# Optimization experiments

Hardware: AMD Instinct MI355X
Metric: run time of the kernel (lower is better)

The kernel has to match this reference:

```python
import jax, jax.numpy as jnp
import numpy as np

B, S, D, H, NS = 4, 2048, 1024, 16, 300
DK = D // H                      # 64
NSP = (NS + H - 1) // H * H      # 304 (padded skills)
DG = NSP // H                    # 19
NEG_FILL = -1e9                  # fp32 path in the torch module


def setup_inputs() -> dict:
    key = jax.random.key(0)
    ks = jax.random.split(key, 12)
    sc = 0.02
    return {
        "context_sequence": jax.random.normal(ks[0], (B, S, D), jnp.float32),
        "value_sequence": jax.random.normal(ks[1], (B, S, NS), jnp.float32),
        "mask": jnp.triu(jnp.ones((S, S), jnp.bool_), k=1),  # causal: True = masked
        # weights stored as [in, out] (math-equivalent to torch's x @ W.T + b)
        "Wq": jax.random.normal(ks[2], (D, D), jnp.float32) * sc,
        "bq": jnp.zeros((D,), jnp.float32),
        "Wk": jax.random.normal(ks[3], (D, D), jnp.float32) * sc,
        "bk": jnp.zeros((D,), jnp.float32),
        "Wv": jax.random.normal(ks[4], (NS, NS), jnp.float32) * sc,
        "bv": jnp.zeros((NS,), jnp.float32),
        "Wg": jax.random.normal(ks[5], (NS, D), jnp.float32) * sc,  # gain_to_context
        "bg": jnp.zeros((D,), jnp.float32),
        "Wo": jax.random.normal(ks[6], (D, D), jnp.float32) * sc,   # output_proj
        "bo": jnp.zeros((D,), jnp.float32),
    }


def reference(context_sequence, value_sequence, mask,
              Wq, bq, Wk, bk, Wv, bv, Wg, bg, Wo, bo):
    b = context_sequence.shape[0]
    orig_dtype = context_sequence.dtype

    # Q, K: [b, H, S, DK]
    Q = (context_sequence @ Wq + bq).reshape(b, -1, H, DK).transpose(0, 2, 1, 3)
    K = (context_sequence @ Wk + bk).reshape(b, -1, H, DK).transpose(0, 2, 1, 3)

    # intrinsic-gain V: project in skill space, zero-pad to NSP, split heads -> [b, H, S, DG]
    V_proj = value_sequence @ Wv + bv
    V_proj = jnp.pad(V_proj, ((0, 0), (0, 0), (0, NSP - NS)))
    V = V_proj.reshape(b, -1, H, DG).transpose(0, 2, 1, 3)

    # fp32 score upcast, scale by sqrt(d_k), mask, cast back, softmax
    scores = jnp.einsum('bhqd,bhkd->bhqk',
                        Q.astype(jnp.float32), K.astype(jnp.float32)) / np.sqrt(DK)
    scores = jnp.where(mask, NEG_FILL, scores).astype(orig_dtype)
    attn = jax.nn.softmax(scores, axis=-1)

    # [b, H, S, DG] -> [b, S, NSP] -> slice to NS
    head_gains = jnp.einsum('bhqk,bhkd->bhqd', attn, V)
    agg = head_gains.transpose(0, 2, 1, 3).reshape(b, -1, NSP)[..., :NS]

    output = agg @ Wg + bg            # gain_to_context
    return output @ Wo + bo           # output_proj (dropout is identity in eval)
```

## Files before the change

kernel.cpp:

```cpp
#include <hip/hip_runtime.h>
#include <hip/hip_bf16.h>

#define MROWS 8192
#define DMODEL 1024
#define SLEN 2048
#define NHEADS 16
#define DKH 64
#define DGH 19
#define NSKILL 300
#define KGPAD 320
#define AGG_LD 320
#define QK_LD 2048
#define VK 320
#define VTN 384

typedef __attribute__((ext_vector_type(8))) short short8;
typedef __attribute__((ext_vector_type(4))) float floatx4;

__device__ __forceinline__ float bf2f(unsigned short u) {
  union { unsigned int i; float f; } cv;
  cv.i = ((unsigned int)u) << 16;
  return cv.f;
}
__device__ __forceinline__ unsigned short f2bf(float f) {
  __hip_bfloat16 h = __float2bfloat16(f);
  unsigned short u;
  __builtin_memcpy(&u, &h, 2);
  return u;
}

__device__ __forceinline__ float exp2hw(float x) {
#if __has_builtin(__builtin_amdgcn_exp2f)
  return __builtin_amdgcn_exp2f(x);
#else
  return __expf(x * 0.6931471805599453f);
#endif
}
__device__ __forceinline__ unsigned int cvt_pk_bf16(float lo, float hi) {
  unsigned int r;
  asm("v_cvt_pk_bf16_f32 %0, %1, %2" : "=v"(r) : "v"(lo), "v"(hi));
  return r;
}

__device__ __forceinline__ void ld8(const float* p, float* v) {
  float4 a = *(const float4*)p;
  float4 b = *((const float4*)p + 1);
  v[0]=a.x; v[1]=a.y; v[2]=a.z; v[3]=a.w;
  v[4]=b.x; v[5]=b.y; v[6]=b.z; v[7]=b.w;
}
__device__ __forceinline__ void st1(float* p, float v) { *p = v; }
__device__ __forceinline__ void st1(__hip_bfloat16* p, float v) {
  unsigned short raw = f2bf(v); __builtin_memcpy(p, &raw, 2);
}
__device__ __forceinline__ void st8(__hip_bfloat16* p, const float* v) {
  ushort4 a, b;
  a.x=f2bf(v[0]); a.y=f2bf(v[1]); a.z=f2bf(v[2]); a.w=f2bf(v[3]);
  b.x=f2bf(v[4]); b.y=f2bf(v[5]); b.z=f2bf(v[6]); b.w=f2bf(v[7]);
  *(ushort4*)p = a;
  *((ushort4*)p + 1) = b;
}

__device__ __forceinline__ void gl_lds16(const void* g, void* l) {
  __builtin_amdgcn_global_load_lds(
      (const __attribute__((address_space(1))) unsigned int*)g,
      (__attribute__((address_space(3))) unsigned int*)l, 16, 0, 0);
}

__global__ __launch_bounds__(256)
void prep_mega_kernel(const float* __restrict__ X,
                      const float* __restrict__ Vin,
                      const float* __restrict__ Wg,
                      const float* __restrict__ bq, const float* __restrict__ bk,
                      const float* __restrict__ bv,
                      const float* __restrict__ Wq, const float* __restrict__ Wk,
                      const float* __restrict__ Wo, const float* __restrict__ Wv,
                      __hip_bfloat16* __restrict__ Xb,
                      __hip_bfloat16* __restrict__ Vb16,
                      __hip_bfloat16* __restrict__ Wgb,
                      float* __restrict__ biasqk, float* __restrict__ biasv,
                      float* __restrict__ z384,
                      __hip_bfloat16* __restrict__ Wtqk,
                      __hip_bfloat16* __restrict__ WoT,
                      __hip_bfloat16* __restrict__ Wvt)
{
  const int bid = blockIdx.x;
  const int t = threadIdx.x;
  if (bid < 8192) {
    int i = (bid * 256 + t) * 4;
    float4 v = *(const float4*)(X + i);
    ushort4 s;
    s.x = f2bf(v.x); s.y = f2bf(v.y); s.z = f2bf(v.z); s.w = f2bf(v.w);
    *(ushort4*)((__hip_bfloat16*)Xb + i) = s;
    return;
  }
  if (bid < 9472) {
    int idx = (bid - 8192) * 256 + t;
    int row = idx / 40;
    int c8  = (idx - row * 40) * 8;
    const float* ip = Vin + (size_t)row * NSKILL + c8;
    float v[8];
    if (c8 + 8 <= NSKILL) {
      ld8(ip, v);
    } else {
      #pragma unroll
      for (int u = 0; u < 8; u++)
        v[u] = (c8 + u < NSKILL) ? ip[u] : 0.f;
    }
    st8(Vb16 + (size_t)row * VK + c8, v);
    return;
  }
  if (bid < 9856) {
    int i4 = ((bid - 9472) * 256 + t) * 4;
    int r = i4 >> 10;
    ushort4 s = {0, 0, 0, 0};
    if (r < NSKILL) {
      float4 v = *(const float4*)(Wg + i4);
      s.x = f2bf(v.x); s.y = f2bf(v.y); s.z = f2bf(v.z); s.w = f2bf(v.w);
    }
    *(ushort4*)((__hip_bfloat16*)Wgb + i4) = s;
    return;
  }
  if (bid == 9856) {
    for (int i = t; i < 1024; i += 256) { biasqk[i] = bq[i]; biasqk[1024 + i] = bk[i]; }
    for (int i = t; i < 384; i += 256) {
      biasv[i] = (i < NSKILL) ? bv[i] : 0.f;
      z384[i] = 0.f;
    }
    return;
  }
  const float* W; __hip_bfloat16* Wt; int K, Nld, Ntrue, Kpad, kx, ny;
  if (bid < 10881)      { int l = bid - 9857;  W=Wq; Wt=Wtqk;            K=1024; Nld=1024; Ntrue=1024; Kpad=1024; kx=l&31; ny=l>>5; }
  else if (bid < 11905) { int l = bid - 10881; W=Wk; Wt=Wtqk+1024*1024;  K=1024; Nld=1024; Ntrue=1024; Kpad=1024; kx=l&31; ny=l>>5; }
  else if (bid < 12929) { int l = bid - 11905; W=Wo; Wt=WoT;             K=1024; Nld=1024; Ntrue=1024; Kpad=1024; kx=l&31; ny=l>>5; }
  else                  { int l = bid - 12929; W=Wv; Wt=Wvt;             K=NSKILL; Nld=NSKILL; Ntrue=NSKILL; Kpad=VK; kx=l%10; ny=l/10; }
  __shared__ float tb[32][33];
  const int k0 = kx * 32;
  const int n0 = ny * 32;
  const int tx = t & 31, ty = t >> 5;
  #pragma unroll
  for (int i = 0; i < 4; i++) {
    int k = k0 + ty + i*8;
    int nn = n0 + tx;
    tb[ty + i*8][tx] = (k < K && nn < Ntrue) ? W[(size_t)k * Nld + nn] : 0.f;
  }
  __syncthreads();
  #pragma unroll
  for (int i = 0; i < 4; i++) {
    int nn = n0 + ty + i*8;
    int kk = k0 + tx;
    st1(Wt + (size_t)nn * Kpad + kk, tb[tx][ty + i*8]);
  }
}

__device__ __forceinline__ void gemm_core(const short* __restrict__ Ag,
                                          const short* __restrict__ Bg,
                                          int lda, int ldb, int K,
                                          int m0, int n0,
                                          short* Al, short* Bl,
                                          int tid, floatx4 (&acc)[4][4])
{
  const int lane = tid & 63;
  const int wave = tid >> 6;
  const int wy = wave >> 1, wx = wave & 1;
  const int n = lane & 15;
  const int quad = lane >> 4;

  for (int k0 = 0; k0 < K; k0 += 64) {
    #pragma unroll
    for (int it = 0; it < 4; it++) {
      int ci = it*256 + tid;
      int r = ci >> 3, c = ci & 7;
      int cs = c ^ (r & 7);
      gl_lds16(Ag + (size_t)(m0 + r) * lda + k0 + cs*8, &Al[ci*8]);
    }
    #pragma unroll
    for (int it = 0; it < 4; it++) {
      int ci = it*256 + tid;
      int r = ci >> 3, c = ci & 7;
      int cs = c ^ (r & 7);
      gl_lds16(Bg + (size_t)(n0 + r) * ldb + k0 + cs*8, &Bl[ci*8]);
    }
    __syncthreads();

    #pragma unroll
    for (int s = 0; s < 2; s++) {
      short8 af[4], bfr[4];
      const int c = s*4 + quad;
      #pragma unroll
      for (int i = 0; i < 4; i++) {
        int r = wy*64 + i*16 + n;
        af[i] = *(const short8*)&Al[(r*8 + (c ^ (r & 7)))*8];
      }
      #pragma unroll
      for (int j = 0; j < 4; j++) {
        int r = wx*64 + j*16 + n;
        bfr[j] = *(const short8*)&Bl[(r*8 + (c ^ (r & 7)))*8];
      }
      #pragma unroll
      for (int i = 0; i < 4; i++)
        #pragma unroll
        for (int j = 0; j < 4; j++)
          acc[i][j] = __builtin_amdgcn_mfma_f32_16x16x32_bf16(af[i], bfr[j], acc[i][j], 0, 0, 0);
    }
    __syncthreads();
  }
}

__global__ __launch_bounds__(256)
void gemm_qk_vt_kernel(const __hip_bfloat16* __restrict__ Xb,
                       const __hip_bfloat16* __restrict__ Wtqk,
                       const float* __restrict__ biasqk,
                       __hip_bfloat16* __restrict__ QKbuf,
                       const __hip_bfloat16* __restrict__ Vb16,
                       const __hip_bfloat16* __restrict__ Wvt,
                       const float* __restrict__ biasv,
                       __hip_bfloat16* __restrict__ VT)
{
  __shared__ __align__(16) short Al[128*64];
  __shared__ __align__(16) short Bl[128*64];
  const int tid = threadIdx.x;
  const int lane = tid & 63;
  const int wave = tid >> 6;
  const int wy = wave >> 1, wx = wave & 1;
  const int n = lane & 15;
  const int quad = lane >> 4;

  floatx4 acc[4][4];
  #pragma unroll
  for (int i = 0; i < 4; i++)
    #pragma unroll
    for (int j = 0; j < 4; j++) acc[i][j] = (floatx4){0.f,0.f,0.f,0.f};

  if (blockIdx.x < 1024) {
    const int bx = blockIdx.x & 15, by = blockIdx.x >> 4;
    const int m0 = by * 128, n0 = bx * 128;
    gemm_core((const short*)Xb, (const short*)Wtqk, DMODEL, DMODEL, DMODEL,
              m0, n0, Al, Bl, tid, acc);
    float bj[4];
    #pragma unroll
    for (int j = 0; j < 4; j++) bj[j] = biasqk[n0 + wx*64 + j*16 + n];
    #pragma unroll
    for (int i = 0; i < 4; i++) {
      #pragma unroll
      for (int r = 0; r < 4; r++) {
        int row = m0 + wy*64 + i*16 + quad*4 + r;
        __hip_bfloat16* cp = QKbuf + (size_t)row * QK_LD;
        #pragma unroll
        for (int j = 0; j < 4; j++) {
          int col = n0 + wx*64 + j*16 + n;
          st1(cp + col, acc[i][j][r] + bj[j]);
        }
      }
    }
  } else {
    const int l = blockIdx.x - 1024;
    const int bx = l % 3, by = l / 3;
    const int m0 = by * 128, n0 = bx * 128;
    gemm_core((const short*)Vb16, (const short*)Wvt, VK, VK, VK,
              m0, n0, Al, Bl, tid, acc);
    float bj[4];
    #pragma unroll
    for (int j = 0; j < 4; j++) bj[j] = biasv[n0 + wx*64 + j*16 + n];
    #pragma unroll
    for (int i = 0; i < 4; i++) {
      int row0 = m0 + wy*64 + i*16 + quad*4;
      int bb = row0 >> 11, rin = row0 & 2047;
      #pragma unroll
      for (int j = 0; j < 4; j++) {
        int col = n0 + wx*64 + j*16 + n;
        ushort4 pk;
        pk.x = f2bf(acc[i][j][0] + bj[j]);
        pk.y = f2bf(acc[i][j][1] + bj[j]);
        pk.z = f2bf(acc[i][j][2] + bj[j]);
        pk.w = f2bf(acc[i][j][3] + bj[j]);
        *(ushort4*)(VT + ((size_t)bb * VTN + col) * SLEN + rin) = pk;
      }
    }
  }
}

__global__ __launch_bounds__(256)
void wgo_bgo_kernel(const __hip_bfloat16* __restrict__ WoT,
                    const __hip_bfloat16* __restrict__ Wgb,
                    const float* __restrict__ z384,
                    __hip_bfloat16* __restrict__ WgoT,
                    const float* __restrict__ bg, const float* __restrict__ Wo,
                    const float* __restrict__ bo, float* __restrict__ bgo)
{
  __shared__ __align__(16) short Al[128*64];
  __shared__ __align__(16) short Bl[128*64];
  const int tid = threadIdx.x;
  if (blockIdx.x < 24) {
    const int lane = tid & 63;
    const int wave = tid >> 6;
    const int wy = wave >> 1, wx = wave & 1;
    const int n = lane & 15;
    const int quad = lane >> 4;
    const int bx = blockIdx.x % 3, by = blockIdx.x / 3;
    const int m0 = by * 128, n0 = bx * 128;
    floatx4 acc[4][4];
    #pragma unroll
    for (int i = 0; i < 4; i++)
      #pragma unroll
      for (int j = 0; j < 4; j++) acc[i][j] = (floatx4){0.f,0.f,0.f,0.f};
    gemm_core((const short*)WoT, (const short*)Wgb, DMODEL, DMODEL, DMODEL,
              m0, n0, Al, Bl, tid, acc);
    float bj[4];
    #pragma unroll
    for (int j = 0; j < 4; j++) bj[j] = z384[n0 + wx*64 + j*16 + n];
    #pragma unroll
    for (int i = 0; i < 4; i++) {
      #pragma unroll
      for (int r = 0; r < 4; r++) {
        int row = m0 + wy*64 + i*16 + quad*4 + r;
        __hip_bfloat16* cp = WgoT + (size_t)row * 384;
        #pragma unroll
        for (int j = 0; j < 4; j++) {
          int col = n0 + wx*64 + j*16 + n;
          st1(cp + col, acc[i][j][r] + bj[j]);
        }
      }
    }
  } else {
    __shared__ float red[256];
    const int c   = tid & 15;
    const int jg  = tid >> 4;
    const int col = (blockIdx.x - 24) * 16 + c;
    float acc = 0.f;
    const int j0 = jg * 64;
    #pragma unroll 8
    for (int j = j0; j < j0 + 64; j++)
      acc = fmaf(bg[j], Wo[(size_t)j * DMODEL + col], acc);
    red[tid] = acc;
    __syncthreads();
    if (jg == 0) {
      float s = 0.f;
      #pragma unroll
      for (int g = 0; g < 16; g++) s += red[g*16 + c];
      bgo[col] = s + bo[col];
    }
  }
}

__global__ __launch_bounds__(256)
void gemm_final_kernel(const __hip_bfloat16* __restrict__ A,
                       const __hip_bfloat16* __restrict__ Bt,
                       const float* __restrict__ bias,
                       float* __restrict__ C)
{
  __shared__ __align__(16) short Al[128*64];
  __shared__ __align__(16) short Bl[128*64];
  const int tid = threadIdx.x;
  const int lane = tid & 63;
  const int wave = tid >> 6;
  const int wy = wave >> 1, wx = wave & 1;
  const int n = lane & 15;
  const int quad = lane >> 4;
  const int m0 = blockIdx.y * 128;
  const int n0 = blockIdx.x * 128;
  floatx4 acc[4][4];
  #pragma unroll
  for (int i = 0; i < 4; i++)
    #pragma unroll
    for (int j = 0; j < 4; j++) acc[i][j] = (floatx4){0.f,0.f,0.f,0.f};
  gemm_core((const short*)A, (const short*)Bt, KGPAD, 384, KGPAD,
            m0, n0, Al, Bl, tid, acc);
  float bj[4];
  #pragma unroll
  for (int j = 0; j < 4; j++) bj[j] = bias[n0 + wx*64 + j*16 + n];
  #pragma unroll
  for (int i = 0; i < 4; i++) {
    #pragma unroll
    for (int r = 0; r < 4; r++) {
      int row = m0 + wy*64 + i*16 + quad*4 + r;
      float* cp = C + (size_t)row * DMODEL;
      #pragma unroll
      for (int j = 0; j < 4; j++) {
        int col = n0 + wx*64 + j*16 + n;
        cp[col] = acc[i][j][r] + bj[j];
      }
    }
  }
}

#define ATT_BM 128
#define ATT_BK 64
#define ATT_GRID (24*64)

__global__ __launch_bounds__(256)
void attn_mfma_kernel(const __hip_bfloat16* __restrict__ Qb,
                      const __hip_bfloat16* __restrict__ Kb,
                      const __hip_bfloat16* __restrict__ VTg,
                      __hip_bfloat16* __restrict__ Agg,
                      float* __restrict__ Pm, float* __restrict__ Pl,
                      float* __restrict__ Po)
{
  __shared__ __align__(16) short Kf[2][64*64];
  __shared__ __align__(16) short Vf[2][32*64];
  __shared__ __align__(16) unsigned int Plds[4][2][2][4][16][4];

  const int tid  = threadIdx.x;
  const int lane = tid & 63;
  const int wave = tid >> 6;
  const int n    = lane & 15;
  const int quad = lane >> 4;

  const int cid = blockIdx.x >> 6;
  const int bh  = blockIdx.x & 63;
  const int h   = bh & 15;
  const int b   = bh >> 4;
  int qt, kt0, nt, mode;
  if (cid == 0)      { qt = 7;       kt0 = 0;  nt = 16; mode = 0; }
  else if (cid <= 8) { qt = cid + 7; kt0 = 0;  nt = 16; mode = 1; }
  else if (cid == 9) { qt = 15;      kt0 = 16; nt = 16; mode = 2; }
  else {
    int e = (cid - 10) >> 1;
    if (((cid - 10) & 1) == 0) { qt = 6 - e;  kt0 = 0;  nt = 14 - 2*e; mode = 0; }
    else                       { qt = 14 - e; kt0 = 16; nt = 14 - 2*e; mode = 2; }
  }
  const int qbase = qt * ATT_BM;
  const size_t bS = (size_t)b * SLEN;

  const float QSCALE = 0.18033688f;
  short8 qf[2][2];
  #pragma unroll
  for (int rf = 0; rf < 2; rf++)
    #pragma unroll
    for (int ks = 0; ks < 2; ks++) {
      const __hip_bfloat16* qp = Qb + (bS + qbase + wave*32 + rf*16 + n) * QK_LD
                                    + h*DKH + ks*32 + quad*8;
      short8 v = *(const short8*)qp;
      #pragma unroll
      for (int e = 0; e < 8; e++) {
        float f = bf2f((unsigned short)v[e]) * QSCALE;
        v[e] = (short)f2bf(f);
      }
      qf[rf][ks] = v;
    }

  const short* kp;
  {
    int f = tid;
    int nn = f & 15, q = (f >> 4) & 3, c = (f >> 6) & 3;
    kp = (const short*)Kb + (bS + kt0*64 + c*16 + nn) * QK_LD + h*DKH + q*8;
  }
  const short* vp;
  {
    int g = tid;
    int vn = g & 15, vq = (g >> 4) & 3, sv = (g >> 6) & 1, cv = g >> 7;
    vp = (const short*)VTg + ((size_t)b * VTN + h*DGH + cv*16 + vn) * SLEN
         + kt0*64 + sv*32 + vq*8;
  }

  floatx4 of[2][2];
  float mrow[2], lrow[2];
  #pragma unroll
  for (int rf = 0; rf < 2; rf++) {
    #pragma unroll
    for (int cv = 0; cv < 2; cv++) of[rf][cv] = (floatx4){0.f,0.f,0.f,0.f};
    mrow[rf] = -1e30f; lrow[rf] = 0.f;
  }

  const int wrow_max = qbase + wave*32 + 31;

  auto stage = [&](int buf) {
    gl_lds16(kp,      &Kf[buf][tid*8]);
    gl_lds16(kp + 32, &Kf[buf][(tid + 256)*8]);
    gl_lds16(vp,      &Vf[buf][tid*8]);
    kp += 64 * QK_LD;
    vp += 64;
  };

  auto compute_tile = [&](int buf, int kbase) {
    if (kbase > wrow_max) return;
    short8 kfr[4][2];
    #pragma unroll
    for (int cf = 0; cf < 4; cf++)
      #pragma unroll
      for (int s = 0; s < 2; s++)
        kfr[cf][s] = *(const short8*)&Kf[buf][((s*4 + cf)*64 + lane)*8];

    floatx4 sf[2][4];
    __builtin_amdgcn_s_setprio(1);
    #pragma unroll
    for (int rf = 0; rf < 2; rf++)
      #pragma unroll
      for (int cf = 0; cf < 4; cf++) {
        floatx4 a2 = (floatx4){0.f,0.f,0.f,0.f};
        a2 = __builtin_amdgcn_mfma_f32_16x16x32_bf16(kfr[cf][0], qf[rf][0], a2, 0, 0, 0);
        a2 = __builtin_amdgcn_mfma_f32_16x16x32_bf16(kfr[cf][1], qf[rf][1], a2, 0, 0, 0);
        sf[rf][cf] = a2;
      }
    __builtin_amdgcn_s_setprio(0);

    #pragma unroll
    for (int rf = 0; rf < 2; rf++) {
      const int qrow = qbase + wave*32 + rf*16 + n;
      if (kbase + 63 > qbase + wave*32 + rf*16) {
        #pragma unroll
        for (int cf = 0; cf < 4; cf++)
          #pragma unroll
          for (int r = 0; r < 4; r++) {
            int key = kbase + cf*16 + quad*4 + r;
            if (key > qrow) sf[rf][cf][r] = -INFINITY;
          }
      }
      float m0 = fmaxf(sf[rf][0][0], sf[rf][0][1]);
      #pragma unroll
      for (int i = 2; i < 16; i += 2)
        m0 = fmaxf(fmaxf(m0, sf[rf][i>>2][i&3]), sf[rf][(i+1)>>2][(i+1)&3]);
      m0 = fmaxf(m0, __shfl_xor(m0, 16));
      m0 = fmaxf(m0, __shfl_xor(m0, 32));
      float mnew = fmaxf(mrow[rf], m0);
      float alpha = exp2hw(mrow[rf] - mnew);
      mrow[rf] = mnew;
      float rs = 0.f;
      #pragma unroll
      for (int cf = 0; cf < 4; cf++)
        #pragma unroll
        for (int r = 0; r < 4; r++) {
          float p = exp2hw(sf[rf][cf][r] - mnew);
          sf[rf][cf][r] = p;
          rs += p;
        }
      rs += __shfl_xor(rs, 16);
      rs += __shfl_xor(rs, 32);
      lrow[rf] = lrow[rf] * alpha + rs;
      #pragma unroll
      for (int cv = 0; cv < 2; cv++)
        #pragma unroll
        for (int r = 0; r < 4; r++) of[rf][cv][r] *= alpha;

      #pragma unroll
      for (int cf = 0; cf < 4; cf++) {
        unsigned int w0 = cvt_pk_bf16(sf[rf][cf][0], sf[rf][cf][1]);
        unsigned int w1 = cvt_pk_bf16(sf[rf][cf][2], sf[rf][cf][3]);
        int s   = cf >> 1;
        int qt2 = 2*(cf & 1) + (quad >> 1);
        int jp  = 2*(quad & 1);
        *(uint2*)&Plds[wave][rf][s][qt2][n][jp] = make_uint2(w0, w1);
      }
    }

    short8 vfr[2][2];
    #pragma unroll
    for (int cv = 0; cv < 2; cv++)
      #pragma unroll
      for (int s = 0; s < 2; s++)
        vfr[cv][s] = *(const short8*)&Vf[buf][((cv*2 + s)*64 + lane)*8];

    __builtin_amdgcn_s_setprio(1);
    #pragma unroll
    for (int rf = 0; rf < 2; rf++) {
      short8 p0 = *(const short8*)&Plds[wave][rf][0][quad][n][0];
      short8 p1 = *(const short8*)&Plds[wave][rf][1][quad][n][0];
      #pragma unroll
      for (int cv = 0; cv < 2; cv++) {
        floatx4 a2 = of[rf][cv];
        a2 = __builtin_amdgcn_mfma_f32_16x16x32_bf16(vfr[cv][0], p0, a2, 0, 0, 0);
        a2 = __builtin_amdgcn_mfma_f32_16x16x32_bf16(vfr[cv][1], p1, a2, 0, 0, 0);
        of[rf][cv] = a2;
      }
    }
    __builtin_amdgcn_s_setprio(0);
  };

  stage(0);
  for (int kt = 0; kt < nt; kt += 2) {
    stage(1);
    asm volatile("s_waitcnt vmcnt(3)" ::: "memory");
    __builtin_amdgcn_s_barrier();
    __builtin_amdgcn_sched_barrier(0);
    compute_tile(0, (kt0 + kt) * ATT_BK);
    __builtin_amdgcn_sched_barrier(0);
    __builtin_amdgcn_s_barrier();

    if (kt + 2 < nt) {
      stage(0);
      asm volatile("s_waitcnt vmcnt(3)" ::: "memory");
    } else {
      asm volatile("s_waitcnt vmcnt(0)" ::: "memory");
    }
    __builtin_amdgcn_s_barrier();
    __builtin_amdgcn_sched_barrier(0);
    compute_tile(1, (kt0 + kt + 1) * ATT_BK);
    __builtin_amdgcn_sched_barrier(0);
    __builtin_amdgcn_s_barrier();
  }

  if (mode == 0) {
    #pragma unroll
    for (int rf = 0; rf < 2; rf++) {
      float inv = 1.f / lrow[rf];
      int row = qbase + wave*32 + rf*16 + n;
      __hip_bfloat16* op = Agg + (bS + row)*AGG_LD + h*DGH;
      #pragma unroll
      for (int cv = 0; cv < 2; cv++)
        #pragma unroll
        for (int r = 0; r < 4; r++) {
          int dim = cv*16 + quad*4 + r;
          if (dim < DGH) st1(op + dim, of[rf][cv][r] * inv);
        }
    }
    if (h == 15) {
      int row = qbase + (tid >> 1);
      int c0 = 304 + (tid & 1) * 8;
      float z[8] = {0.f,0.f,0.f,0.f,0.f,0.f,0.f,0.f};
      st8(Agg + (bS + row)*AGG_LD + c0, z);
    }
  } else {
    const int p = (qt - 8) * 64 + bh;
    const int sl = mode - 1;
    #pragma unroll
    for (int rf = 0; rf < 2; rf++) {
      int rowl = wave*32 + rf*16 + n;
      size_t ri = (size_t)(sl*512 + p)*128 + rowl;
      float* po = Po + ri*20;
      #pragma unroll
      for (int cv = 0; cv < 2; cv++)
        #pragma unroll
        for (int r = 0; r < 4; r++) {
          int dim = cv*16 + quad*4 + r;
          if (dim < DGH) po[dim] = of[rf][cv][r];
        }
      if (quad == 0) { Pm[ri] = mrow[rf]; Pl[ri] = lrow[rf]; }
    }
  }
}

__global__ __launch_bounds__(256)
void attn_combine_kernel(const float* __restrict__ Pm, const float* __restrict__ Pl,
                         const float* __restrict__ Po,
                         __hip_bfloat16* __restrict__ Agg)
{
  int idx = blockIdx.x * 256 + threadIdx.x;
  int p = idx >> 7, rowl = idx & 127;
  int qt = 8 + (p >> 6), bh = p & 63, h = bh & 15, b = bh >> 4;
  size_t riA = (size_t)p*128 + rowl;
  size_t riB = (size_t)(512 + p)*128 + rowl;
  float mA = Pm[riA], mB = Pm[riB];
  float lA = Pl[riA], lB = Pl[riB];
  float m = fmaxf(mA, mB);
  float wA = exp2hw(mA - m), wB = exp2hw(mB - m);
  float inv = 1.f / (wA*lA + wB*lB);
  wA *= inv; wB *= inv;
  const float* oA = Po + riA*20;
  const float* oB = Po + riB*20;
  size_t row = (size_t)b*SLEN + qt*128 + rowl;
  __hip_bfloat16* op = Agg + row*AGG_LD + h*DGH;
  #pragma unroll
  for (int d = 0; d < DGH; d++)
    st1(op + d, wA*oA[d] + wB*oB[d]);
  if (h == 15) {
    uint4 z = {0,0,0,0};
    *(uint4*)(Agg + row*AGG_LD + 304) = z;
    *(uint4*)(Agg + row*AGG_LD + 312) = z;
  }
}

extern "C" void kernel_launch(void* const* d_in, const int* in_sizes, int n_in,
                              void* d_out, int out_size, void* d_ws, size_t ws_size,
                              hipStream_t stream) {
  const float* X   = (const float*)d_in[0];
  const float* Vin = (const float*)d_in[1];
  const float* Wq  = (const float*)d_in[3];
  const float* bq  = (const float*)d_in[4];
  const float* Wk  = (const float*)d_in[5];
  const float* bk  = (const float*)d_in[6];
  const float* Wv  = (const float*)d_in[7];
  const float* bv  = (const float*)d_in[8];
  const float* Wg  = (const float*)d_in[9];
  const float* bg  = (const float*)d_in[10];
  const float* Wo  = (const float*)d_in[11];
  const float* bo  = (const float*)d_in[12];
  float* out = (float*)d_out;

  char* ws = (char*)d_ws;
  __hip_bfloat16* Xb    = (__hip_bfloat16*)(ws);
  __hip_bfloat16* AggB  = (__hip_bfloat16*)(ws);
  __hip_bfloat16* WgoT  = (__hip_bfloat16*)(ws + 12582912);
  float*          bgoW  = (float*)         (ws + 13369344);
  __hip_bfloat16* QKbuf = (__hip_bfloat16*)(ws + 16777216);
  __hip_bfloat16* WoT   = (__hip_bfloat16*)(ws + 50331648);

  char* ob = (char*)d_out;
  __hip_bfloat16* Wtqk   = (__hip_bfloat16*)(ob);
  float*          biasqk = (float*)(ob + 4194304);
  __hip_bfloat16* Vb16   = (__hip_bfloat16*)(ob + 4202496);
  float*          biasv  = (float*)(ob + 9445376);
  float*          z384   = (float*)(ob + 9446912);
  __hip_bfloat16* Wgb    = (__hip_bfloat16*)(ob + 9448448);
  __hip_bfloat16* Wvt    = (__hip_bfloat16*)(ob + 10234880);
  float*          Pm     = (float*)(ob);
  float*          Pl     = (float*)(ob + 524288);
  float*          Po     = (float*)(ob + 1048576);
  __hip_bfloat16* VT     = (__hip_bfloat16*)(ob + 12582912);

  dim3 blk(256);
  prep_mega_kernel<<<dim3(13049), blk, 0, stream>>>(
      X, Vin, Wg, bq, bk, bv, Wq, Wk, Wo, Wv,
      Xb, Vb16, Wgb, biasqk, biasv, z384, Wtqk, WoT, Wvt);

  gemm_qk_vt_kernel<<<dim3(1216), blk, 0, stream>>>(
      Xb, Wtqk, biasqk, QKbuf, Vb16, Wvt, biasv, VT);

  wgo_bgo_kernel<<<dim3(88), blk, 0, stream>>>(
      WoT, Wgb, z384, WgoT, bg, Wo, bo, bgoW);

  attn_mfma_kernel<<<dim3(ATT_GRID), dim3(256), 0, stream>>>(
      QKbuf, QKbuf + 1024, VT, AggB, Pm, Pl, Po);

  attn_combine_kernel<<<dim3(256), blk, 0, stream>>>(Pm, Pl, Po, AggB);

  gemm_final_kernel<<<dim3(8, 64), blk, 0, stream>>>(AggB, WgoT, bgoW, out);
}
```

Baseline: 279.9 us.

## Single-buffer attention LDS tiles and raise occupancy via launch bounds

```diff
diff --git a/kernel.cpp b/kernel.cpp
--- a/kernel.cpp
+++ b/kernel.cpp
@@ -387,7 +387,7 @@
 #define ATT_BK 64
 #define ATT_GRID (24*64)
 
-__global__ __launch_bounds__(256)
+__global__ __launch_bounds__(256, 7)
 void attn_mfma_kernel(const __hip_bfloat16* __restrict__ Qb,
                       const __hip_bfloat16* __restrict__ Kb,
                       const __hip_bfloat16* __restrict__ VTg,
@@ -395,9 +395,9 @@
                       float* __restrict__ Pm, float* __restrict__ Pl,
                       float* __restrict__ Po)
 {
-  __shared__ __align__(16) short Kf[2][64*64];
-  __shared__ __align__(16) short Vf[2][32*64];
-  __shared__ __align__(16) unsigned int Plds[4][2][2][4][16][4];
+  __shared__ __align__(16) short Kf[64*64];
+  __shared__ __align__(16) short Vf[32*64];
+  __shared__ __align__(16) unsigned int Plds[4][2][4][16][4];
 
   const int tid  = threadIdx.x;
   const int lane = tid & 63;
@@ -463,22 +463,22 @@
 
   const int wrow_max = qbase + wave*32 + 31;
 
-  auto stage = [&](int buf) {
-    gl_lds16(kp,      &Kf[buf][tid*8]);
-    gl_lds16(kp + 32, &Kf[buf][(tid + 256)*8]);
-    gl_lds16(vp,      &Vf[buf][tid*8]);
+  auto stage = [&]() {
+    gl_lds16(kp,      &Kf[tid*8]);
+    gl_lds16(kp + 32, &Kf[(tid + 256)*8]);
+    gl_lds16(vp,      &Vf[tid*8]);
     kp += 64 * QK_LD;
     vp += 64;
   };
 
-  auto compute_tile = [&](int buf, int kbase) {
+  auto compute_tile = [&](int kbase) {
     if (kbase > wrow_max) return;
     short8 kfr[4][2];
     #pragma unroll
     for (int cf = 0; cf < 4; cf++)
       #pragma unroll
       for (int s = 0; s < 2; s++)
-        kfr[cf][s] = *(const short8*)&Kf[buf][((s*4 + cf)*64 + lane)*8];
+        kfr[cf][s] = *(const short8*)&Kf[((s*4 + cf)*64 + lane)*8];
 
     floatx4 sf[2][4];
     __builtin_amdgcn_s_setprio(1);
@@ -492,6 +492,13 @@
         sf[rf][cf] = a2;
       }
     __builtin_amdgcn_s_setprio(0);
+
+    short8 vfr[2][2];
+    #pragma unroll
+    for (int cv = 0; cv < 2; cv++)
+      #pragma unroll
+      for (int s = 0; s < 2; s++)
+        vfr[cv][s] = *(const short8*)&Vf[((cv*2 + s)*64 + lane)*8];
 
     #pragma unroll
     for (int rf = 0; rf < 2; rf++) {
@@ -538,22 +545,11 @@
         int s   = cf >> 1;
         int qt2 = 2*(cf & 1) + (quad >> 1);
         int jp  = 2*(quad & 1);
-        *(uint2*)&Plds[wave][rf][s][qt2][n][jp] = make_uint2(w0, w1);
-      }
-    }
-
-    short8 vfr[2][2];
-    #pragma unroll
-    for (int cv = 0; cv < 2; cv++)
-      #pragma unroll
-      for (int s = 0; s < 2; s++)
-        vfr[cv][s] = *(const short8*)&Vf[buf][((cv*2 + s)*64 + lane)*8];
-
-    __builtin_amdgcn_s_setprio(1);
-    #pragma unroll
-    for (int rf = 0; rf < 2; rf++) {
-      short8 p0 = *(const short8*)&Plds[wave][rf][0][quad][n][0];
-      short8 p1 = *(const short8*)&Plds[wave][rf][1][quad][n][0];
+        *(uint2*)&Plds[wave][s][qt2][n][jp] = make_uint2(w0, w1);
+      }
+      short8 p0 = *(const short8*)&Plds[wave][0][quad][n][0];
+      short8 p1 = *(const short8*)&Plds[wave][1][quad][n][0];
+      __builtin_amdgcn_s_setprio(1);
       #pragma unroll
       for (int cv = 0; cv < 2; cv++) {
         floatx4 a2 = of[rf][cv];
@@ -561,31 +557,15 @@
         a2 = __builtin_amdgcn_mfma_f32_16x16x32_bf16(vfr[cv][1], p1, a2, 0, 0, 0);
         of[rf][cv] = a2;
       }
-    }
-    __builtin_amdgcn_s_setprio(0);
+      __builtin_amdgcn_s_setprio(0);
+    }
   };
 
-  stage(0);
-  for (int kt = 0; kt < nt; kt += 2) {
-    stage(1);
-    asm volatile("s_waitcnt vmcnt(3)" ::: "memory");
-    __builtin_amdgcn_s_barrier();
-    __builtin_amdgcn_sched_barrier(0);
-    compute_tile(0, (kt0 + kt) * ATT_BK);
-    __builtin_amdgcn_sched_barrier(0);
-    __builtin_amdgcn_s_barrier();
-
-    if (kt + 2 < nt) {
-      stage(0);
-      asm volatile("s_waitcnt vmcnt(3)" ::: "memory");
-    } else {
-      asm volatile("s_waitcnt vmcnt(0)" ::: "memory");
-    }
-    __builtin_amdgcn_s_barrier();
-    __builtin_amdgcn_sched_barrier(0);
-    compute_tile(1, (kt0 + kt + 1) * ATT_BK);
-    __builtin_amdgcn_sched_barrier(0);
-    __builtin_amdgcn_s_barrier();
+  for (int kt = 0; kt < nt; kt++) {
+    stage();
+    __syncthreads();
+    compute_tile((kt0 + kt) * ATT_BK);
+    __syncthreads();
   }
 
   if (mode == 0) {
```

Result: slower. 496.6 us (+77.5%).
